# Kernel optimization log

Measured on AMD Instinct MI355X. Metric: run time of the kernel, lower is better.

Reference implementation:

```python
import jax, jax.numpy as jnp
import numpy as np

B, S, D_MODEL, D_HIDDEN = 4, 2048, 1024, 4096

# --- BitNet b1.58-style quantizers (STE in bwd version) ---

def act_quant(x):
    # per-token int8 absmax quantization over last dim
    scale = 127.0 / jnp.clip(jnp.max(jnp.abs(x), axis=-1, keepdims=True), 1e-5)
    return jnp.clip(jnp.round(x * scale), -128, 127) / scale

def weight_quant(w):
    # ternary weights with global mean-abs scale
    scale = 1.0 / jnp.clip(jnp.mean(jnp.abs(w)), 1e-5)
    return jnp.clip(jnp.round(w * scale), -1, 1) / scale

def bit_linear(x, w):
    # STE: forward uses quantized values, gradient passes through
    xq = x + jax.lax.stop_gradient(act_quant(x) - x)
    wq = w + jax.lax.stop_gradient(weight_quant(w) - w)
    return jnp.einsum('bsd,hd->bsh', xq, wq)

def depthwise_conv1d(x_bcl, w, b):
    # x_bcl: [B, C, L], w: [C, 1, 3], b: [C]
    y = jax.lax.conv_general_dilated(
        x_bcl, w, window_strides=(1,), padding=[(1, 1)],
        dimension_numbers=('NCH', 'OIH', 'NCH'),
        feature_group_count=x_bcl.shape[1])
    return y + b[None, :, None]


def setup_inputs() -> dict:
    key = jax.random.key(0)
    ks = jax.random.split(key, 5)
    lim1 = 1.0 / np.sqrt(D_MODEL)
    lim2 = 1.0 / np.sqrt(D_HIDDEN)
    limc = 1.0 / np.sqrt(3.0)  # fan_in = 1*3 for depthwise conv
    return {
        'x': jax.random.normal(ks[0], (B, S, D_MODEL), dtype=jnp.float32),
        'w1': jax.random.uniform(ks[1], (D_HIDDEN, D_MODEL), jnp.float32, -lim1, lim1),
        'conv_w': jax.random.uniform(ks[2], (D_HIDDEN, 1, 3), jnp.float32, -limc, limc),
        'conv_b': jax.random.uniform(ks[3], (D_HIDDEN,), jnp.float32, -limc, limc),
        'w2': jax.random.uniform(ks[4], (D_MODEL, D_HIDDEN), jnp.float32, -lim2, lim2),
    }


def reference(x, w1, conv_w, conv_b, w2):
    h = bit_linear(x, w1)                      # [B, S, H]
    h = depthwise_conv1d(h.transpose(0, 2, 1), conv_w, conv_b)  # [B, H, S]
    h = h.transpose(0, 2, 1)                   # [B, S, H]
    h = jax.nn.silu(h)
    return bit_linear(h, w2)                   # [B, S, D]
```

## Files before the change

### kernel.cpp

```cpp
#include <hip/hip_runtime.h>
#include <cstdint>

#define S_    2048
#define DM    1024
#define DH    4096
#define NTOK  8192
#define WELEM 4194304
#define CT    8

typedef int v4i __attribute__((ext_vector_type(4)));
typedef _Float16 half8 __attribute__((ext_vector_type(8)));
typedef char char8v __attribute__((ext_vector_type(8)));

#define GLOAD_LDS16(g, l)                                                   \
    __builtin_amdgcn_global_load_lds(                                       \
        (const __attribute__((address_space(1))) void*)(g),                 \
        (__attribute__((address_space(3))) void*)(l), 16, 0, 0)

static __device__ __forceinline__ void sbar() {
    asm volatile("" ::: "memory");
    __builtin_amdgcn_s_barrier();
    asm volatile("" ::: "memory");
}
#define LGKM0() asm volatile("s_waitcnt lgkmcnt(0)" ::: "memory")
#define VMC0() asm volatile("s_waitcnt vmcnt(0)" ::: "memory")
#define VMC3() asm volatile("s_waitcnt vmcnt(3)" ::: "memory")
#define VMC4() asm volatile("s_waitcnt vmcnt(4)" ::: "memory")
#define VMC8() asm volatile("s_waitcnt vmcnt(8)" ::: "memory")

__global__ __launch_bounds__(256) void absmean_partial(const float4* __restrict__ wa,
                                                       const float4* __restrict__ wb,
                                                       double* __restrict__ partial) {
    __shared__ double red[256];
    const float4* w = (blockIdx.x < 1024) ? wa : wb;
    int base = (blockIdx.x & 1023) * 1024;
    double s = 0.0;
#pragma unroll
    for (int k = 0; k < 4; ++k) {
        float4 v = w[base + (k << 8) + threadIdx.x];
        s += (double)fabsf(v.x) + (double)fabsf(v.y) +
             (double)fabsf(v.z) + (double)fabsf(v.w);
    }
    red[threadIdx.x] = s;
    __syncthreads();
    for (int off = 128; off > 0; off >>= 1) {
        if (threadIdx.x < off) red[threadIdx.x] += red[threadIdx.x + off];
        __syncthreads();
    }
    if (threadIdx.x == 0) partial[blockIdx.x] = red[0];
}

__global__ __launch_bounds__(256) void finalize_scales(const double* __restrict__ part,
                                                       float* __restrict__ sc) {
    __shared__ double red[1024];
#pragma unroll 1
    for (int m = 0; m < 2; ++m) {
        const double* p = part + m * 1024;
        __syncthreads();
#pragma unroll
        for (int k = 0; k < 4; ++k) red[(k << 8) + threadIdx.x] = p[(k << 8) + threadIdx.x];
        __syncthreads();
        double s = red[threadIdx.x] + red[threadIdx.x + 256] +
                   red[threadIdx.x + 512] + red[threadIdx.x + 768];
        __syncthreads();
        red[threadIdx.x] = s;
        __syncthreads();
        for (int off = 128; off > 0; off >>= 1) {
            if (threadIdx.x < off) red[threadIdx.x] += red[threadIdx.x + off];
            __syncthreads();
        }
        if (threadIdx.x == 0) {
            double mean = red[0] / (double)WELEM;
            float mf = fmaxf((float)mean, 1e-5f);
            float scale = 1.0f / mf;
            sc[2 * m]     = scale;
            sc[2 * m + 1] = 1.0f / scale;
        }
    }
}

__global__ __launch_bounds__(256) void quant_all(const float4* __restrict__ w1,
                                                 const float4* __restrict__ w2,
                                                 const float4* __restrict__ x,
                                                 char4* __restrict__ qw1,
                                                 char4* __restrict__ qw2,
                                                 char4* __restrict__ qx,
                                                 float* __restrict__ dqx,
                                                 const float* __restrict__ sc) {
    __shared__ float red[256];
    if (blockIdx.x < 8192) {
        bool second = blockIdx.x >= 4096;
        const float4* w = second ? w2 : w1;
        char4* q = second ? qw2 : qw1;
        float scale = sc[second ? 2 : 0];
        int i = (blockIdx.x & 4095) * 256 + threadIdx.x;
        float4 v = w[i];
        char4 o;
        o.x = (signed char)(int)fminf(fmaxf(rintf(v.x * scale), -1.f), 1.f);
        o.y = (signed char)(int)fminf(fmaxf(rintf(v.y * scale), -1.f), 1.f);
        o.z = (signed char)(int)fminf(fmaxf(rintf(v.z * scale), -1.f), 1.f);
        o.w = (signed char)(int)fminf(fmaxf(rintf(v.w * scale), -1.f), 1.f);
        q[i] = o;
    } else {
        int t = blockIdx.x - 8192;
        float4 v = x[(size_t)t * 256 + threadIdx.x];
        float mx = fmaxf(fmaxf(fabsf(v.x), fabsf(v.y)), fmaxf(fabsf(v.z), fabsf(v.w)));
        red[threadIdx.x] = mx;
        __syncthreads();
        for (int off = 128; off > 0; off >>= 1) {
            if (threadIdx.x < off) red[threadIdx.x] = fmaxf(red[threadIdx.x], red[threadIdx.x + off]);
            __syncthreads();
        }
        float scale = 127.0f / fmaxf(red[0], 1e-5f);
        char4 o;
        o.x = (signed char)(int)rintf(v.x * scale);
        o.y = (signed char)(int)rintf(v.y * scale);
        o.z = (signed char)(int)rintf(v.z * scale);
        o.w = (signed char)(int)rintf(v.w * scale);
        qx[(size_t)t * 256 + threadIdx.x] = o;
        if (threadIdx.x == 0) dqx[t] = 1.0f / scale;
    }
}

__global__ __launch_bounds__(512) void conv_silu_quant(const half8* __restrict__ h,
                                                       const float4* __restrict__ cwv,
                                                       const float4* __restrict__ cbv,
                                                       char8v* __restrict__ q,
                                                       float* __restrict__ dq) {
    __shared__ float red[2][8];
    const int tid = threadIdx.x;
    const int t0 = blockIdx.x * CT;
    const int s0 = t0 & (S_ - 1);

    float wc[24], bs[8];
    {
        float4 tmp;
#pragma unroll
        for (int i = 0; i < 6; ++i) {
            tmp = cwv[tid * 6 + i];
            wc[4 * i] = tmp.x; wc[4 * i + 1] = tmp.y; wc[4 * i + 2] = tmp.z; wc[4 * i + 3] = tmp.w;
        }
        tmp = cbv[tid * 2];     bs[0] = tmp.x; bs[1] = tmp.y; bs[2] = tmp.z; bs[3] = tmp.w;
        tmp = cbv[tid * 2 + 1]; bs[4] = tmp.x; bs[5] = tmp.y; bs[6] = tmp.z; bs[7] = tmp.w;
    }

    auto ldrow = [&](int t, bool valid, float* dst) {
        if (valid) {
            half8 raw = h[(size_t)t * 512 + tid];
#pragma unroll
            for (int e = 0; e < 8; ++e) dst[e] = (float)raw[e];
        } else {
#pragma unroll
            for (int e = 0; e < 8; ++e) dst[e] = 0.f;
        }
    };

    float pv[8], cu[8], nx[8], pf[8];
    ldrow(t0 - 1, s0 > 0, pv);
    ldrow(t0, true, cu);
    ldrow(t0 + 1, true, nx);

#pragma unroll
    for (int i = 0; i < CT; ++i) {
        const int t = t0 + i;
        ldrow(t + 2, (s0 + i + 2) < S_, pf);

        float v[8];
        float mx = 0.f;
#pragma unroll
        for (int e = 0; e < 8; ++e) {
            float y = wc[3 * e] * pv[e] + wc[3 * e + 1] * cu[e] + wc[3 * e + 2] * nx[e] + bs[e];
            float ex = __builtin_amdgcn_exp2f(-1.44269504088896f * y);
            float r  = y * __builtin_amdgcn_rcpf(1.0f + ex);
            v[e] = r;
            mx = fmaxf(mx, fabsf(r));
        }
#pragma unroll
        for (int off = 32; off > 0; off >>= 1)
            mx = fmaxf(mx, __shfl_down(mx, off, 64));
        if ((tid & 63) == 0) red[i & 1][tid >> 6] = mx;
        __syncthreads();
        float rmax = red[i & 1][0];
#pragma unroll
        for (int w = 1; w < 8; ++w) rmax = fmaxf(rmax, red[i & 1][w]);
        float scale = 127.0f / fmaxf(rmax, 1e-5f);
        char8v o;
#pragma unroll
        for (int e = 0; e < 8; ++e)
            o[e] = (signed char)(int)rintf(v[e] * scale);
        q[(size_t)t * 512 + tid] = o;
        if (tid == 0) dq[t] = 1.0f / scale;
#pragma unroll
        for (int e = 0; e < 8; ++e) { pv[e] = cu[e]; cu[e] = nx[e]; nx[e] = pf[e]; }
    }
}

__global__ __launch_bounds__(512, 2)
void gemm1_8ph(const int8_t* __restrict__ A, const int8_t* __restrict__ Bm,
               _Float16* __restrict__ C, const float* __restrict__ rowdq,
               const float* __restrict__ sc, int slot, int N, int K) {
    __shared__ __align__(16) int8_t lds[4][32768];
    const int tid  = threadIdx.x;
    const int lane = tid & 63;
    const int wave = tid >> 6;

    const int nwg = gridDim.x * gridDim.y;
    int flat = blockIdx.y * gridDim.x + blockIdx.x;
    flat = (flat & 7) * (nwg >> 3) + (flat >> 3);
    const int bx = flat % gridDim.x;
    const int by = flat / gridDim.x;
    const int mbase = by << 8;
    const int nbase = bx << 8;
    const int NT = K >> 6;

    const int wm = wave >> 2;
    const int wn = wave & 3;

    const int srow = lane >> 2;
    const int csrc = (((lane & 3) ^ ((lane >> 3) & 3)) << 4);
    const int8_t* Ag = A  + (size_t)(mbase + wave * 32 + srow) * K + csrc;
    const int8_t* Bg = Bm + (size_t)(nbase + wave * 32 + srow) * K + csrc;

    auto stageA = [&](int s, int tt) {
        const size_t ko = (size_t)tt << 6;
        int8_t* d = &lds[s][wave << 11];
        GLOAD_LDS16(Ag + ko,                  d);
        GLOAD_LDS16(Ag + ko + (size_t)16 * K, d + 1024);
    };
    auto stageB = [&](int s, int tt) {
        const size_t ko = (size_t)tt << 6;
        int8_t* d = &lds[s][16384 + (wave << 11)];
        GLOAD_LDS16(Bg + ko,                  d);
        GLOAD_LDS16(Bg + ko + (size_t)16 * K, d + 1024);
    };

    const int fc   = (((lane >> 4) ^ ((lane >> 1) & 3)) << 4);
    const int aoff = ((wm * 128 + (lane & 15)) << 6) + fc;
    const int boff = 16384 + ((wn * 64 + (lane & 15)) << 6) + fc;

    v4i acc[8][4] = {};

    stageA(0, 0); stageB(0, 0);
    if (NT > 1) { stageA(1, 1); stageB(1, 1); }
    if (NT > 2) { stageA(2, 2); stageB(2, 2); }
    if (NT > 2)      VMC8();
    else if (NT > 1) VMC4();
    else             VMC0();
    sbar();

    for (int t = 0; t < NT; ++t) {
        const int8_t* base = &lds[t & 3][0];
        const int s3 = (t + 3) & 3;

        v4i bf[4], af[4];
#pragma unroll
        for (int j = 0; j < 4; ++j)
            bf[j] = *reinterpret_cast<const v4i*>(base + boff + (j << 10));
#pragma unroll
        for (int i = 0; i < 4; ++i)
            af[i] = *reinterpret_cast<const v4i*>(base + aoff + (i << 10));
        if (t + 3 < NT) stageA(s3, t + 3);
        sbar();
        LGKM0();
        __builtin_amdgcn_s_setprio(1);
#pragma unroll
        for (int i = 0; i < 4; ++i)
#pragma unroll
            for (int j = 0; j < 4; ++j)
                acc[i][j] = __builtin_amdgcn_mfma_i32_16x16x64_i8(af[i], bf[j], acc[i][j], 0, 0, 0);
        __builtin_amdgcn_s_setprio(0);
        sbar();

#pragma unroll
        for (int i = 0; i < 4; ++i)
            af[i] = *reinterpret_cast<const v4i*>(base + aoff + ((i + 4) << 10));
        if (t + 3 < NT) stageB(s3, t + 3);
        sbar();
        LGKM0();
        __builtin_amdgcn_s_setprio(1);
#pragma unroll
        for (int i = 0; i < 4; ++i)
#pragma unroll
            for (int j = 0; j < 4; ++j)
                acc[i + 4][j] = __builtin_amdgcn_mfma_i32_16x16x64_i8(af[i], bf[j], acc[i + 4][j], 0, 0, 0);
        __builtin_amdgcn_s_setprio(0);

        if (t + 3 < NT)      VMC8();
        else if (t + 2 < NT) VMC4();
        else if (t + 1 < NT) VMC0();
        sbar();
    }

    const float wdq = sc[slot];
    const int quad = lane >> 4;
    const int col  = lane & 15;
#pragma unroll
    for (int i = 0; i < 8; ++i) {
#pragma unroll
        for (int r = 0; r < 4; ++r) {
            int m = mbase + (wm << 7) + (i << 4) + (quad << 2) + r;
            float rs = rowdq[m] * wdq;
#pragma unroll
            for (int j = 0; j < 4; ++j) {
                int n = nbase + (wn << 6) + (j << 4) + col;
                C[(size_t)m * N + n] = (_Float16)((float)acc[i][j][r] * rs);
            }
        }
    }
}

template <int BM, int WAVES, typename OutT>
__global__ __launch_bounds__(WAVES * 64, (BM == 256) ? 4 : 3)
void gemm_i8_bk64(const int8_t* __restrict__ A, const int8_t* __restrict__ Bm,
                  OutT* __restrict__ C, const float* __restrict__ rowdq,
                  const float* __restrict__ sc, int slot, int N, int K) {
    constexpr int BN = 128;
    constexpr int ABYTES = BM * 64;
    constexpr int BUF = (BM + BN) * 64;
    constexpr int ALOADS = BM / 16 / WAVES;
    constexpr int BLOADS = BN / 16 / WAVES;
    constexpr int L = ALOADS + BLOADS;

    __shared__ __align__(16) int8_t lds[3][BUF];
    const int tid  = threadIdx.x;
    const int lane = tid & 63;
    const int wave = tid >> 6;

    const int nwg = gridDim.x * gridDim.y;
    int flat = blockIdx.y * gridDim.x + blockIdx.x;
    flat = (flat & 7) * (nwg >> 3) + (flat >> 3);
    const int bx = flat % gridDim.x;
    const int by = flat / gridDim.x;
    const int mbase = by * BM;
    const int nbase = bx << 7;
    const int NT = K >> 6;

    const int wm = wave >> 1;
    const int wn = wave & 1;

    const int srow = lane >> 2;
    const int csrc = (((lane & 3) ^ ((lane >> 3) & 3)) << 4);
    const int8_t* Ag = A  + (size_t)(mbase + wave * (ALOADS * 16) + srow) * K + csrc;
    const int8_t* Bg = Bm + (size_t)(nbase + wave * (BLOADS * 16) + srow) * K + csrc;

    auto stage = [&](int s, int tt) {
        const size_t ko = (size_t)tt << 6;
        int8_t* dA = &lds[s][(wave * ALOADS) << 10];
        int8_t* dB = &lds[s][ABYTES + ((wave * BLOADS) << 10)];
#pragma unroll
        for (int l = 0; l < ALOADS; ++l)
            GLOAD_LDS16(Ag + ko + (size_t)(l * 16) * K, dA + (l << 10));
#pragma unroll
        for (int l = 0; l < BLOADS; ++l)
            GLOAD_LDS16(Bg + ko + (size_t)(l * 16) * K, dB + (l << 10));
    };

    const int fc   = (((lane >> 4) ^ ((lane >> 1) & 3)) << 4);
    const int aoff = ((wm * 64 + (lane & 15)) << 6) + fc;
    const int boff = ABYTES + ((wn * 64 + (lane & 15)) << 6) + fc;

    v4i acc[4][4] = {};

    stage(0, 0);
    stage(1, 1);
    if constexpr (L == 3) VMC3(); else VMC4();
    sbar();

    int sb = 0;
    for (int t = 0; t < NT; ++t) {
        const int8_t* base = &lds[sb][0];
        v4i af[4], bf[4];
#pragma unroll
        for (int i = 0; i < 4; ++i)
            af[i] = *reinterpret_cast<const v4i*>(base + aoff + (i << 10));
#pragma unroll
        for (int j = 0; j < 4; ++j)
            bf[j] = *reinterpret_cast<const v4i*>(base + boff + (j << 10));
        int s2 = sb + 2; if (s2 >= 3) s2 -= 3;
        if (t + 2 < NT) stage(s2, t + 2);

        __builtin_amdgcn_s_setprio(1);
#pragma unroll
        for (int i = 0; i < 4; ++i)
#pragma unroll
            for (int j = 0; j < 4; ++j)
                acc[i][j] = __builtin_amdgcn_mfma_i32_16x16x64_i8(af[i], bf[j], acc[i][j], 0, 0, 0);
        __builtin_amdgcn_s_setprio(0);

        if (t + 2 < NT)      { if constexpr (L == 3) VMC3(); else VMC4(); }
        else if (t + 1 < NT) VMC0();
        sbar();
        if (++sb == 3) sb = 0;
    }

    const float wdq = sc[slot];
    const int quad = lane >> 4;
    const int col  = lane & 15;
#pragma unroll
    for (int i = 0; i < 4; ++i) {
#pragma unroll
        for (int r = 0; r < 4; ++r) {
            int m = mbase + (wm << 6) + (i << 4) + (quad << 2) + r;
            float rs = rowdq[m] * wdq;
#pragma unroll
            for (int j = 0; j < 4; ++j) {
                int n = nbase + (wn << 6) + (j << 4) + col;
                C[(size_t)m * N + n] = (OutT)((float)acc[i][j][r] * rs);
            }
        }
    }
}

extern "C" void kernel_launch(void* const* d_in, const int* in_sizes, int n_in,
                              void* d_out, int out_size, void* d_ws, size_t ws_size,
                              hipStream_t stream) {
    const float* x  = (const float*)d_in[0];
    const float* w1 = (const float*)d_in[1];
    const float* cw = (const float*)d_in[2];
    const float* cb = (const float*)d_in[3];
    const float* w2 = (const float*)d_in[4];
    float* out = (float*)d_out;
    char* ws = (char*)d_ws;

    double* part  = (double*)(ws + 0);
    float*  sc    = (float*)(ws + 16384);
    float*  dqx   = (float*)(ws + 16640);
    float*  dqh   = (float*)(ws + 49408);
    int8_t* qw1   = (int8_t*)(ws + 82176);
    int8_t* qw2   = (int8_t*)(ws + 4276480);
    int8_t* qx    = (int8_t*)(ws + 8470784);
    int8_t* qh    = (int8_t*)(ws + 16859392);
    _Float16* h   = (_Float16*)(ws + 50413824);

    absmean_partial<<<2048, 256, 0, stream>>>((const float4*)w1, (const float4*)w2, part);
    finalize_scales<<<1, 256, 0, stream>>>(part, sc);
    quant_all<<<16384, 256, 0, stream>>>((const float4*)w1, (const float4*)w2,
                                         (const float4*)x, (char4*)qw1, (char4*)qw2,
                                         (char4*)qx, dqx, sc);

    dim3 g1(DH / 256, NTOK / 256);
    gemm1_8ph<<<g1, 512, 0, stream>>>(qx, qw1, h, dqx, sc, 1, DH, DM);

    conv_silu_quant<<<NTOK / CT, 512, 0, stream>>>((const half8*)h, (const float4*)cw,
                                                   (const float4*)cb, (char8v*)qh, dqh);

    dim3 g2(DM / 128, NTOK / 128);
    gemm_i8_bk64<128, 4, float><<<g2, 256, 0, stream>>>(qh, qw2, out, dqh, sc, 3, DM, DH);
}
```

Baseline: 234.5 us.

## Restructure GEMM1 to BK=128 double-buffered pipeline with split half-stage loads

Replaces the 4-stage BK=64 ring buffer in the first int8 GEMM with a 2-buffer scheme where each buffer holds a 128-wide K tile as two 64-wide halves. Each half of the next tile is prefetched while the current tile's halves are consumed, which halves the loop-iteration count and reduces the per-iteration control overhead. Prefetch depth drops from three tiles ahead to roughly one, so global-memory latency may be hidden less well. LDS use stays at 128KB per block.

```diff
diff --git a/kernel.cpp b/kernel.cpp
--- a/kernel.cpp
+++ b/kernel.cpp
@@ -26,7 +26,6 @@
 #define VMC0() asm volatile("s_waitcnt vmcnt(0)" ::: "memory")
 #define VMC3() asm volatile("s_waitcnt vmcnt(3)" ::: "memory")
 #define VMC4() asm volatile("s_waitcnt vmcnt(4)" ::: "memory")
-#define VMC8() asm volatile("s_waitcnt vmcnt(8)" ::: "memory")
 
 __global__ __launch_bounds__(256) void absmean_partial(const float4* __restrict__ wa,
                                                        const float4* __restrict__ wb,
@@ -196,10 +195,10 @@
 }
 
 __global__ __launch_bounds__(512, 2)
-void gemm1_8ph(const int8_t* __restrict__ A, const int8_t* __restrict__ Bm,
-               _Float16* __restrict__ C, const float* __restrict__ rowdq,
-               const float* __restrict__ sc, int slot, int N, int K) {
-    __shared__ __align__(16) int8_t lds[4][32768];
+void gemm1_bk128(const int8_t* __restrict__ A, const int8_t* __restrict__ Bm,
+                 _Float16* __restrict__ C, const float* __restrict__ rowdq,
+                 const float* __restrict__ sc, int slot, int N, int K) {
+    __shared__ __align__(16) int8_t lds[2][65536];
     const int tid  = threadIdx.x;
     const int lane = tid & 63;
     const int wave = tid >> 6;
@@ -211,7 +210,7 @@
     const int by = flat / gridDim.x;
     const int mbase = by << 8;
     const int nbase = bx << 8;
-    const int NT = K >> 6;
+    const int NT = K >> 7;
 
     const int wm = wave >> 2;
     const int wn = wave & 3;
@@ -221,45 +220,41 @@
     const int8_t* Ag = A  + (size_t)(mbase + wave * 32 + srow) * K + csrc;
     const int8_t* Bg = Bm + (size_t)(nbase + wave * 32 + srow) * K + csrc;
 
-    auto stageA = [&](int s, int tt) {
-        const size_t ko = (size_t)tt << 6;
-        int8_t* d = &lds[s][wave << 11];
-        GLOAD_LDS16(Ag + ko,                  d);
-        GLOAD_LDS16(Ag + ko + (size_t)16 * K, d + 1024);
+    auto stage = [&](int b, int s, int tt) {
+        const size_t ko = ((size_t)tt << 7) + ((size_t)s << 6);
+        int8_t* dA = &lds[b][(s << 14) + (wave << 11)];
+        int8_t* dB = &lds[b][32768 + (s << 14) + (wave << 11)];
+        GLOAD_LDS16(Ag + ko,                  dA);
+        GLOAD_LDS16(Ag + ko + (size_t)16 * K, dA + 1024);
+        GLOAD_LDS16(Bg + ko,                  dB);
+        GLOAD_LDS16(Bg + ko + (size_t)16 * K, dB + 1024);
     };
-    auto stageB = [&](int s, int tt) {
-        const size_t ko = (size_t)tt << 6;
-        int8_t* d = &lds[s][16384 + (wave << 11)];
-        GLOAD_LDS16(Bg + ko,                  d);
-        GLOAD_LDS16(Bg + ko + (size_t)16 * K, d + 1024);
-    };
-
-    const int fc   = (((lane >> 4) ^ ((lane >> 1) & 3)) << 4);
-    const int aoff = ((wm * 128 + (lane & 15)) << 6) + fc;
-    const int boff = 16384 + ((wn * 64 + (lane & 15)) << 6) + fc;
+
+    const int fc    = (((lane >> 4) ^ ((lane >> 1) & 3)) << 4);
+    const int abase = ((wm * 128 + (lane & 15)) << 6) + fc;
+    const int bbase = 32768 + ((wn * 64 + (lane & 15)) << 6) + fc;
 
     v4i acc[8][4] = {};
 
-    stageA(0, 0); stageB(0, 0);
-    if (NT > 1) { stageA(1, 1); stageB(1, 1); }
-    if (NT > 2) { stageA(2, 2); stageB(2, 2); }
-    if (NT > 2)      VMC8();
-    else if (NT > 1) VMC4();
-    else             VMC0();
+    stage(0, 0, 0);
+    stage(0, 1, 0);
+    VMC4();
     sbar();
 
     for (int t = 0; t < NT; ++t) {
-        const int8_t* base = &lds[t & 3][0];
-        const int s3 = (t + 3) & 3;
+        const int8_t* base = &lds[t & 1][0];
+        const int nb = (t & 1) ^ 1;
+        const bool pf = (t + 1 < NT);
 
         v4i bf[4], af[4];
+
 #pragma unroll
         for (int j = 0; j < 4; ++j)
-            bf[j] = *reinterpret_cast<const v4i*>(base + boff + (j << 10));
-#pragma unroll
-        for (int i = 0; i < 4; ++i)
-            af[i] = *reinterpret_cast<const v4i*>(base + aoff + (i << 10));
-        if (t + 3 < NT) stageA(s3, t + 3);
+            bf[j] = *reinterpret_cast<const v4i*>(base + bbase + (j << 10));
+#pragma unroll
+        for (int i = 0; i < 4; ++i)
+            af[i] = *reinterpret_cast<const v4i*>(base + abase + (i << 10));
+        if (pf) stage(nb, 0, t + 1);
         sbar();
         LGKM0();
         __builtin_amdgcn_s_setprio(1);
@@ -273,8 +268,7 @@
 
 #pragma unroll
         for (int i = 0; i < 4; ++i)
-            af[i] = *reinterpret_cast<const v4i*>(base + aoff + ((i + 4) << 10));
-        if (t + 3 < NT) stageB(s3, t + 3);
+            af[i] = *reinterpret_cast<const v4i*>(base + abase + ((i + 4) << 10));
         sbar();
         LGKM0();
         __builtin_amdgcn_s_setprio(1);
@@ -284,10 +278,40 @@
             for (int j = 0; j < 4; ++j)
                 acc[i + 4][j] = __builtin_amdgcn_mfma_i32_16x16x64_i8(af[i], bf[j], acc[i + 4][j], 0, 0, 0);
         __builtin_amdgcn_s_setprio(0);
-
-        if (t + 3 < NT)      VMC8();
-        else if (t + 2 < NT) VMC4();
-        else if (t + 1 < NT) VMC0();
+        if (pf) VMC4(); else VMC0();
+        sbar();
+
+#pragma unroll
+        for (int j = 0; j < 4; ++j)
+            bf[j] = *reinterpret_cast<const v4i*>(base + 16384 + bbase + (j << 10));
+#pragma unroll
+        for (int i = 0; i < 4; ++i)
+            af[i] = *reinterpret_cast<const v4i*>(base + 16384 + abase + (i << 10));
+        if (pf) stage(nb, 1, t + 1);
+        sbar();
+        LGKM0();
+        __builtin_amdgcn_s_setprio(1);
+#pragma unroll
+        for (int i = 0; i < 4; ++i)
+#pragma unroll
+            for (int j = 0; j < 4; ++j)
+                acc[i][j] = __builtin_amdgcn_mfma_i32_16x16x64_i8(af[i], bf[j], acc[i][j], 0, 0, 0);
+        __builtin_amdgcn_s_setprio(0);
+        sbar();
+
+#pragma unroll
+        for (int i = 0; i < 4; ++i)
+            af[i] = *reinterpret_cast<const v4i*>(base + 16384 + abase + ((i + 4) << 10));
+        sbar();
+        LGKM0();
+        __builtin_amdgcn_s_setprio(1);
+#pragma unroll
+        for (int i = 0; i < 4; ++i)
+#pragma unroll
+            for (int j = 0; j < 4; ++j)
+                acc[i + 4][j] = __builtin_amdgcn_mfma_i32_16x16x64_i8(af[i], bf[j], acc[i + 4][j], 0, 0, 0);
+        __builtin_amdgcn_s_setprio(0);
+        if (pf) VMC4();
         sbar();
     }
 
@@ -439,7 +463,7 @@
                                          (char4*)qx, dqx, sc);
 
     dim3 g1(DH / 256, NTOK / 256);
-    gemm1_8ph<<<g1, 512, 0, stream>>>(qx, qw1, h, dqx, sc, 1, DH, DM);
+    gemm1_bk128<<<g1, 512, 0, stream>>>(qx, qw1, h, dqx, sc, 1, DH, DM);
 
     conv_silu_quant<<<NTOK / CT, 512, 0, stream>>>((const half8*)h, (const float4*)cw,
                                                    (const float4*)cb, (char8v*)qh, dqh);
```

New measurement: 233.2 us. No clear change (-0.5%).

## Load GEMM1 B operand directly to registers, stage only A through LDS

Applied to the files above, without the earlier changes.

The first int8 GEMM stops staging the weight (B) tile through LDS. Each wave now loads its B fragments straight from global memory into registers, double-buffered across k-steps, while A keeps an LDS ring of depth two ahead. This halves LDS usage and drops one barrier phase per k-step, so LDS traffic and sync overhead go down. In exchange, B rows are loaded redundantly by the waves that share a column slice, global traffic per block rises, and register pressure grows because of the extra B buffers and eight A fragments held at once.

```diff
diff --git a/kernel.cpp b/kernel.cpp
--- a/kernel.cpp
+++ b/kernel.cpp
@@ -22,11 +22,12 @@
     __builtin_amdgcn_s_barrier();
     asm volatile("" ::: "memory");
 }
+#define FENCE() asm volatile("" ::: "memory")
 #define LGKM0() asm volatile("s_waitcnt lgkmcnt(0)" ::: "memory")
 #define VMC0() asm volatile("s_waitcnt vmcnt(0)" ::: "memory")
 #define VMC3() asm volatile("s_waitcnt vmcnt(3)" ::: "memory")
 #define VMC4() asm volatile("s_waitcnt vmcnt(4)" ::: "memory")
-#define VMC8() asm volatile("s_waitcnt vmcnt(8)" ::: "memory")
+#define VMC6() asm volatile("s_waitcnt vmcnt(6)" ::: "memory")
 
 __global__ __launch_bounds__(256) void absmean_partial(const float4* __restrict__ wa,
                                                        const float4* __restrict__ wb,
@@ -196,10 +197,10 @@
 }
 
 __global__ __launch_bounds__(512, 2)
-void gemm1_8ph(const int8_t* __restrict__ A, const int8_t* __restrict__ Bm,
-               _Float16* __restrict__ C, const float* __restrict__ rowdq,
-               const float* __restrict__ sc, int slot, int N, int K) {
-    __shared__ __align__(16) int8_t lds[4][32768];
+void gemm1_bdir(const int8_t* __restrict__ A, const int8_t* __restrict__ Bm,
+                _Float16* __restrict__ C, const float* __restrict__ rowdq,
+                const float* __restrict__ sc, int slot, int N, int K) {
+    __shared__ __align__(16) int8_t lds[4][16384];
     const int tid  = threadIdx.x;
     const int lane = tid & 63;
     const int wave = tid >> 6;
@@ -218,77 +219,62 @@
 
     const int srow = lane >> 2;
     const int csrc = (((lane & 3) ^ ((lane >> 3) & 3)) << 4);
-    const int8_t* Ag = A  + (size_t)(mbase + wave * 32 + srow) * K + csrc;
-    const int8_t* Bg = Bm + (size_t)(nbase + wave * 32 + srow) * K + csrc;
-
-    auto stageA = [&](int s, int tt) {
+    const int8_t* Ag = A + (size_t)(mbase + wave * 32 + srow) * K + csrc;
+
+    auto stageA = [&](int b, int tt) {
         const size_t ko = (size_t)tt << 6;
-        int8_t* d = &lds[s][wave << 11];
+        int8_t* d = &lds[b][wave << 11];
         GLOAD_LDS16(Ag + ko,                  d);
         GLOAD_LDS16(Ag + ko + (size_t)16 * K, d + 1024);
     };
-    auto stageB = [&](int s, int tt) {
+
+    const int8_t* Bg = Bm + (size_t)(nbase + wn * 64 + (lane & 15)) * K
+                          + ((lane >> 4) << 4);
+    auto loadB = [&](v4i (&bf)[4], int tt) {
         const size_t ko = (size_t)tt << 6;
-        int8_t* d = &lds[s][16384 + (wave << 11)];
-        GLOAD_LDS16(Bg + ko,                  d);
-        GLOAD_LDS16(Bg + ko + (size_t)16 * K, d + 1024);
+#pragma unroll
+        for (int j = 0; j < 4; ++j)
+            bf[j] = *reinterpret_cast<const v4i*>(Bg + ko + (size_t)(j * 16) * K);
     };
 
     const int fc   = (((lane >> 4) ^ ((lane >> 1) & 3)) << 4);
     const int aoff = ((wm * 128 + (lane & 15)) << 6) + fc;
-    const int boff = 16384 + ((wn * 64 + (lane & 15)) << 6) + fc;
 
     v4i acc[8][4] = {};
-
-    stageA(0, 0); stageB(0, 0);
-    if (NT > 1) { stageA(1, 1); stageB(1, 1); }
-    if (NT > 2) { stageA(2, 2); stageB(2, 2); }
-    if (NT > 2)      VMC8();
-    else if (NT > 1) VMC4();
-    else             VMC0();
+    v4i bf0[4], bf1[4];
+
+    stageA(0, 0);
+    stageA(1, 1);
+    FENCE();
+    loadB(bf0, 0);
+    VMC4();
     sbar();
 
-    for (int t = 0; t < NT; ++t) {
+    auto tile = [&](int t, v4i (&bc)[4], v4i (&bn)[4]) {
         const int8_t* base = &lds[t & 3][0];
-        const int s3 = (t + 3) & 3;
-
-        v4i bf[4], af[4];
-#pragma unroll
-        for (int j = 0; j < 4; ++j)
-            bf[j] = *reinterpret_cast<const v4i*>(base + boff + (j << 10));
-#pragma unroll
-        for (int i = 0; i < 4; ++i)
+        v4i af[8];
+#pragma unroll
+        for (int i = 0; i < 8; ++i)
             af[i] = *reinterpret_cast<const v4i*>(base + aoff + (i << 10));
-        if (t + 3 < NT) stageA(s3, t + 3);
-        sbar();
+        if (t + 1 < NT) loadB(bn, t + 1);
+        if (t + 2 < NT) stageA((t + 2) & 3, t + 2);
         LGKM0();
+        if (t + 2 < NT)      VMC6();
+        else if (t + 1 < NT) VMC4();
+        else                 VMC0();
         __builtin_amdgcn_s_setprio(1);
 #pragma unroll
-        for (int i = 0; i < 4; ++i)
+        for (int i = 0; i < 8; ++i)
 #pragma unroll
             for (int j = 0; j < 4; ++j)
-                acc[i][j] = __builtin_amdgcn_mfma_i32_16x16x64_i8(af[i], bf[j], acc[i][j], 0, 0, 0);
+                acc[i][j] = __builtin_amdgcn_mfma_i32_16x16x64_i8(af[i], bc[j], acc[i][j], 0, 0, 0);
         __builtin_amdgcn_s_setprio(0);
         sbar();
-
-#pragma unroll
-        for (int i = 0; i < 4; ++i)
-            af[i] = *reinterpret_cast<const v4i*>(base + aoff + ((i + 4) << 10));
-        if (t + 3 < NT) stageB(s3, t + 3);
-        sbar();
-        LGKM0();
-        __builtin_amdgcn_s_setprio(1);
-#pragma unroll
-        for (int i = 0; i < 4; ++i)
-#pragma unroll
-            for (int j = 0; j < 4; ++j)
-                acc[i + 4][j] = __builtin_amdgcn_mfma_i32_16x16x64_i8(af[i], bf[j], acc[i + 4][j], 0, 0, 0);
-        __builtin_amdgcn_s_setprio(0);
-
-        if (t + 3 < NT)      VMC8();
-        else if (t + 2 < NT) VMC4();
-        else if (t + 1 < NT) VMC0();
-        sbar();
+    };
+
+    for (int t = 0; t < NT; t += 2) {
+        tile(t,     bf0, bf1);
+        tile(t + 1, bf1, bf0);
     }
 
     const float wdq = sc[slot];
@@ -439,7 +425,7 @@
                                          (char4*)qx, dqx, sc);
 
     dim3 g1(DH / 256, NTOK / 256);
-    gemm1_8ph<<<g1, 512, 0, stream>>>(qx, qw1, h, dqx, sc, 1, DH, DM);
+    gemm1_bdir<<<g1, 512, 0, stream>>>(qx, qw1, h, dqx, sc, 1, DH, DM);
 
     conv_silu_quant<<<NTOK / CT, 512, 0, stream>>>((const half8*)h, (const float4*)cw,
                                                    (const float4*)cb, (char8v*)qh, dqh);
```

Result: slower. 245.2 us (+4.6%).
